# Kernel optimization log

Hardware: AMD Instinct MI355X
Metric: run time of the kernel (lower is better)

The kernel has to match this reference:

```python
import jax, jax.numpy as jnp
import numpy as np

N_NODES = 20000   # N
N_EDGES = 320000  # E (avg degree 16)
T_STEPS = 16      # T
IN_FEATS = 1      # F
HG = 64           # hidden_g
HT = 128          # hidden_t
LN_EPS = 1e-5


def _layer_norm(x, g, b):
    mu = jnp.mean(x, axis=-1, keepdims=True)
    var = jnp.mean((x - mu) ** 2, axis=-1, keepdims=True)
    return (x - mu) * jax.lax.rsqrt(var + LN_EPS) * g + b


def setup_inputs() -> dict:
    key = jax.random.key(0)
    k = jax.random.split(key, 16)
    r = lambda i, shape, s: jax.random.normal(k[i], shape, jnp.float32) * s
    return dict(
        x_seq=jax.random.normal(k[0], (1, T_STEPS, N_NODES, IN_FEATS), jnp.float32),
        edge_index=jax.random.randint(k[1], (2, N_EDGES), 0, N_NODES, dtype=jnp.int32),
        # SAGEConv layer 0: lin_l (aggregated neighbors, has bias) + lin_r (root)
        W_l0=r(2, (IN_FEATS, HG), 0.5), W_r0=r(3, (IN_FEATS, HG), 0.5), b0=jnp.zeros((HG,), jnp.float32),
        ln0_g=jnp.ones((HG,), jnp.float32), ln0_b=jnp.zeros((HG,), jnp.float32),
        # SAGEConv layer 1
        W_l1=r(4, (HG, HG), 0.1), W_r1=r(5, (HG, HG), 0.1), b1=jnp.zeros((HG,), jnp.float32),
        ln1_g=jnp.ones((HG,), jnp.float32), ln1_b=jnp.zeros((HG,), jnp.float32),
        # GRU (torch layout: gates r,z,n stacked along first dim)
        gru_Wih=r(6, (3 * HT, HG), 0.05), gru_Whh=r(7, (3 * HT, HT), 0.05),
        gru_bih=jnp.zeros((3 * HT,), jnp.float32), gru_bhh=jnp.zeros((3 * HT,), jnp.float32),
        # head
        head_W=r(8, (HT, 1), 0.05), head_b=jnp.zeros((1,), jnp.float32),
    )


def reference(x_seq, edge_index, W_l0, W_r0, b0, ln0_g, ln0_b,
              W_l1, W_r1, b1, ln1_g, ln1_b,
              gru_Wih, gru_Whh, gru_bih, gru_bhh, head_W, head_b):
    src, dst = edge_index[0], edge_index[1]
    # in-degree for mean aggregation (clamped to 1, like PyG mean aggr on isolated nodes)
    deg = jnp.clip(jax.ops.segment_sum(jnp.ones((N_EDGES,), jnp.float32), dst,
                                       num_segments=N_NODES), 1.0)[:, None]

    def sage(x, Wl, Wr, b):
        # mean over incoming neighbors, then lin_l(aggr) + lin_r(root)
        agg = jax.ops.segment_sum(x[src], dst, num_segments=N_NODES) / deg
        return agg @ Wl + x @ Wr + b

    def stack(xt):  # xt: (N, F) -> (N, HG); dropout is identity in eval mode
        h = jax.nn.relu(_layer_norm(sage(xt, W_l0, W_r0, b0), ln0_g, ln0_b))
        h = jax.nn.relu(_layer_norm(sage(h, W_l1, W_r1, b1), ln1_g, ln1_b))
        return h

    X = x_seq[0]  # (T, N, F), B == 1
    # scan over timesteps (matches the per-t Python loop, bounds peak memory)
    _, H = jax.lax.scan(lambda c, xt: (c, stack(xt)), None, X)  # H: (T, N, HG)

    def gru_step(h, xt):  # torch GRU cell; batch = N nodes
        gi = xt @ gru_Wih.T + gru_bih
        gh = h @ gru_Whh.T + gru_bhh
        ir, iz, inn = jnp.split(gi, 3, axis=-1)
        hr, hz, hn = jnp.split(gh, 3, axis=-1)
        r = jax.nn.sigmoid(ir + hr)
        z = jax.nn.sigmoid(iz + hz)
        n = jnp.tanh(inn + r * hn)
        return (1.0 - z) * n + z * h, None

    h0 = jnp.zeros((N_NODES, HT), x_seq.dtype)
    hT, _ = jax.lax.scan(gru_step, h0, H)
    y = (hT @ head_W + head_b)[:, 0]  # (N,)
    return y
```

## Files before the change

### kernel.cpp

```cpp
#include <hip/hip_runtime.h>
#include <math.h>

#define NN 20000
#define NE 320000
#define TS 16
#define HG 64
#define HTT 128
#define NG 384
#define LN_EPS 1e-5f
#define ASTR 1032

typedef __attribute__((ext_vector_type(8))) _Float16 f16x8;
typedef __attribute__((ext_vector_type(4))) float f32x4;

__device__ __forceinline__ float wave_sum64(float v) {
  #pragma unroll
  for (int off = 32; off > 0; off >>= 1) v += __shfl_xor(v, off, 64);
  return v;
}
__device__ __forceinline__ float quad_sum16(float v) {
  #pragma unroll
  for (int off = 1; off < 16; off <<= 1) v += __shfl_xor(v, off, 64);
  return v;
}
__device__ __forceinline__ float fast_sigmoid(float x) {
  return __builtin_amdgcn_rcpf(1.f + __expf(-x));
}
__device__ __forceinline__ float fast_tanh(float x) {
  float e = __expf(-2.f * fabsf(x));
  float th = (1.f - e) * __builtin_amdgcn_rcpf(1.f + e);
  return copysignf(th, x);
}

__global__ __launch_bounds__(256) void k_setup(
    const float* __restrict__ x_seq, float* __restrict__ xT,
    const float* __restrict__ Wih, _Float16* __restrict__ WihF,
    const float* __restrict__ Whh, _Float16* __restrict__ WhhF,
    const float* __restrict__ Wl1, const float* __restrict__ Wr1,
    _Float16* __restrict__ Wchi, _Float16* __restrict__ Wclo,
    const float* __restrict__ Wl0, const float* __restrict__ Wr0,
    const float* __restrict__ b0, const float* __restrict__ g0,
    const float* __restrict__ be0, float* __restrict__ P,
    int* __restrict__ cnt) {
  int gid = blockIdx.x * 256 + threadIdx.x;
  int stride = gridDim.x * 256;
  for (int i = gid; i < NN * TS; i += stride) {
    int t = i / NN, n = i - t * NN;
    xT[n * 16 + t] = x_seq[i];
  }
  for (int i = gid; i < NG * HG; i += stride) WihF[i] = (_Float16)Wih[i];
  for (int i = gid; i < NG * HTT; i += stride) WhhF[i] = (_Float16)Whh[i];
  for (int i = gid; i < HG * 128; i += stride) {
    int n = i >> 7, k = i & 127;
    float x = (k < HG) ? Wl1[k * HG + n] : Wr1[(k - HG) * HG + n];
    _Float16 h = (_Float16)x;
    Wchi[i] = h;
    Wclo[i] = (_Float16)(x - (float)h);
  }
  for (int i = gid; i < NN; i += stride) cnt[i] = 0;
  if (blockIdx.x == 0 && threadIdx.x < 64) {
    int f = threadIdx.x;
    float u = Wl0[f], v = Wr0[f], c = b0[f], g = g0[f];
    float um = wave_sum64(u) * (1.f / 64.f);
    float vm = wave_sum64(v) * (1.f / 64.f);
    float cm = wave_sum64(c) * (1.f / 64.f);
    float uc = u - um, vc = v - vm, cc = c - cm;
    float muu = wave_sum64(uc * uc) * (1.f / 64.f);
    float mvv = wave_sum64(vc * vc) * (1.f / 64.f);
    float mcc = wave_sum64(cc * cc) * (1.f / 64.f);
    float muv = wave_sum64(uc * vc) * (1.f / 64.f);
    float muc = wave_sum64(uc * cc) * (1.f / 64.f);
    float mvc = wave_sum64(vc * cc) * (1.f / 64.f);
    P[f] = uc * g; P[64 + f] = vc * g; P[128 + f] = cc * g; P[192 + f] = be0[f];
    if (f == 0) {
      P[256] = muu; P[257] = mvv; P[258] = mcc;
      P[259] = muv; P[260] = muc; P[261] = mvc;
    }
  }
}

__global__ void k_hist(const int* __restrict__ dst, int* cnt) {
  int e = blockIdx.x * blockDim.x + threadIdx.x;
  if (e < NE) atomicAdd(&cnt[dst[e]], 1);
}

__global__ void k_scan(int* cnt, int* row_ptr, float* deg_inv) {
  __shared__ int s[1024];
  const int PER = 20;
  int tid = threadIdx.x;
  int base = tid * PER;
  int vloc[PER], dloc[PER];
  int sum = 0;
  #pragma unroll
  for (int j = 0; j < PER; j++) {
    int n = base + j;
    int d = (n < NN) ? cnt[n] : 0;
    vloc[j] = sum;
    dloc[j] = d;
    sum += d;
  }
  s[tid] = sum;
  __syncthreads();
  for (int off = 1; off < 1024; off <<= 1) {
    int t = (tid >= off) ? s[tid - off] : 0;
    __syncthreads();
    s[tid] += t;
    __syncthreads();
  }
  int excl = s[tid] - sum;
  #pragma unroll
  for (int j = 0; j < PER; j++) {
    int n = base + j;
    if (n < NN) {
      int rp = excl + vloc[j];
      row_ptr[n] = rp;
      cnt[n] = rp;
      int d = dloc[j];
      deg_inv[n] = 1.0f / (float)((d > 1) ? d : 1);
    }
  }
  if (tid == 1023) row_ptr[NN] = s[1023];
}

__global__ void k_fill(const int* __restrict__ src, const int* __restrict__ dst,
                       int* cursor, int* col) {
  int e = blockIdx.x * blockDim.x + threadIdx.x;
  if (e < NE) {
    int p = atomicAdd(&cursor[dst[e]], 1);
    col[p] = src[e];
  }
}

__global__ __launch_bounds__(256) void k_h0_fused(
    const float* __restrict__ xT,
    const int* __restrict__ row_ptr, const int* __restrict__ col,
    const float* __restrict__ deg_inv,
    const float* __restrict__ P,
    _Float16* __restrict__ h0r) {
  int lane = threadIdx.x & 63;
  int n = blockIdx.x * 4 + (threadIdx.x >> 6);
  int grp = lane >> 4, tl = lane & 15;
  int beg = row_ptr[n];
  int deg = row_ptr[n + 1] - beg;
  float s0 = 0.f, s1 = 0.f;
  int iters = (deg + 7) >> 3;
  for (int it = 0; it < iters; it++) {
    int e0 = it * 8 + grp, e1 = it * 8 + 4 + grp;
    bool v0 = e0 < deg, v1 = e1 < deg;
    int i0 = v0 ? e0 : 0, i1 = v1 ? e1 : 0;
    int c0 = col[beg + i0];
    int c1 = col[beg + i1];
    float x0 = xT[c0 * 16 + tl];
    float x1 = xT[c1 * 16 + tl];
    s0 += v0 ? x0 : 0.f;
    s1 += v1 ? x1 : 0.f;
  }
  float s = s0 + s1;
  s += __shfl_xor(s, 16, 64);
  s += __shfl_xor(s, 32, 64);
  float aggv = s * deg_inv[n];
  float xv = xT[n * 16 + tl];
  float muu = P[256], mvv = P[257], mcc = P[258];
  float muv = P[259], muc = P[260], mvc = P[261];
  #pragma unroll
  for (int half = 0; half < 2; half++) {
    int c = lane + half * 64;
    int t = c >> 3, f8 = (c & 7) * 8;
    float a = __shfl(aggv, t, 64);
    float x = __shfl(xv, t, 64);
    float var = a * a * muu + x * x * mvv + mcc
              + 2.f * (a * x * muv + a * muc + x * mvc);
    float rstd = rsqrtf(var + LN_EPS);
    f16x8 o;
    #pragma unroll
    for (int j = 0; j < 8; j++) {
      int f = f8 + j;
      float d = a * P[f] + x * P[64 + f] + P[128 + f];
      o[j] = (_Float16)fmaxf(d * rstd + P[192 + f], 0.f);
    }
    *(f16x8*)&h0r[(size_t)n * 1024 + c * 8] = o;
  }
}

__global__ __launch_bounds__(256) void k_sage_fused(
    const _Float16* __restrict__ h0r,
    const int* __restrict__ row_ptr, const int* __restrict__ col,
    const float* __restrict__ deg_inv,
    const _Float16* __restrict__ Wchi, const _Float16* __restrict__ Wclo,
    const float* __restrict__ b1, const float* __restrict__ g1, const float* __restrict__ be1,
    _Float16* __restrict__ Ht_all) {
  __shared__ _Float16 aggL[16 * ASTR];
  int tid = threadIdx.x;
  int lane = tid & 63, wave = tid >> 6;
  int col16 = lane & 15, quad = lane >> 4;
  int m0 = blockIdx.x * 16;

  for (int i = 0; i < 4; i++) {
    int nl = wave * 4 + i;
    int n = m0 + nl;
    int beg = row_ptr[n];
    int deg = row_ptr[n + 1] - beg;
    const f16x8 z = {0,0,0,0,0,0,0,0};
    f16x8 aH0 = z, aH1 = z, aH2 = z, aH3 = z;
    f16x8 aL0 = z, aL1 = z, aL2 = z, aL3 = z;
    int e = 0;
    for (; e + 8 <= deg; e += 8) {
      int c0 = col[beg + e + 0], c1 = col[beg + e + 1];
      int c2 = col[beg + e + 2], c3 = col[beg + e + 3];
      int c4 = col[beg + e + 4], c5 = col[beg + e + 5];
      int c6 = col[beg + e + 6], c7 = col[beg + e + 7];
      const f16x8* p0 = (const f16x8*)(h0r + (size_t)c0 * 1024);
      const f16x8* p1 = (const f16x8*)(h0r + (size_t)c1 * 1024);
      const f16x8* p2 = (const f16x8*)(h0r + (size_t)c2 * 1024);
      const f16x8* p3 = (const f16x8*)(h0r + (size_t)c3 * 1024);
      const f16x8* p4 = (const f16x8*)(h0r + (size_t)c4 * 1024);
      const f16x8* p5 = (const f16x8*)(h0r + (size_t)c5 * 1024);
      const f16x8* p6 = (const f16x8*)(h0r + (size_t)c6 * 1024);
      const f16x8* p7 = (const f16x8*)(h0r + (size_t)c7 * 1024);
      f16x8 d0a = p0[lane], d0b = p0[lane + 64];
      f16x8 d1a = p1[lane], d1b = p1[lane + 64];
      f16x8 d2a = p2[lane], d2b = p2[lane + 64];
      f16x8 d3a = p3[lane], d3b = p3[lane + 64];
      f16x8 d4a = p4[lane], d4b = p4[lane + 64];
      f16x8 d5a = p5[lane], d5b = p5[lane + 64];
      f16x8 d6a = p6[lane], d6b = p6[lane + 64];
      f16x8 d7a = p7[lane], d7b = p7[lane + 64];
      aH0 += d0a; aL0 += d0b;
      aH1 += d1a; aL1 += d1b;
      aH2 += d2a; aL2 += d2b;
      aH3 += d3a; aL3 += d3b;
      aH0 += d4a; aL0 += d4b;
      aH1 += d5a; aL1 += d5b;
      aH2 += d6a; aL2 += d6b;
      aH3 += d7a; aL3 += d7b;
    }
    for (; e + 4 <= deg; e += 4) {
      int c0 = col[beg + e + 0], c1 = col[beg + e + 1];
      int c2 = col[beg + e + 2], c3 = col[beg + e + 3];
      const f16x8* p0 = (const f16x8*)(h0r + (size_t)c0 * 1024);
      const f16x8* p1 = (const f16x8*)(h0r + (size_t)c1 * 1024);
      const f16x8* p2 = (const f16x8*)(h0r + (size_t)c2 * 1024);
      const f16x8* p3 = (const f16x8*)(h0r + (size_t)c3 * 1024);
      f16x8 d0a = p0[lane], d0b = p0[lane + 64];
      f16x8 d1a = p1[lane], d1b = p1[lane + 64];
      f16x8 d2a = p2[lane], d2b = p2[lane + 64];
      f16x8 d3a = p3[lane], d3b = p3[lane + 64];
      aH0 += d0a; aL0 += d0b;
      aH1 += d1a; aL1 += d1b;
      aH2 += d2a; aL2 += d2b;
      aH3 += d3a; aL3 += d3b;
    }
    for (; e < deg; e++) {
      int c = col[beg + e];
      const f16x8* p = (const f16x8*)(h0r + (size_t)c * 1024);
      aH0 += p[lane]; aL0 += p[lane + 64];
    }
    float di = deg_inv[n];
    f16x8 o0, o1;
    #pragma unroll
    for (int j = 0; j < 8; j++) {
      o0[j] = (_Float16)((((float)aH0[j] + (float)aH1[j]) +
                          ((float)aH2[j] + (float)aH3[j])) * di);
      o1[j] = (_Float16)((((float)aL0[j] + (float)aL1[j]) +
                          ((float)aL2[j] + (float)aL3[j])) * di);
    }
    *(f16x8*)&aggL[nl * ASTR + lane * 8] = o0;
    *(f16x8*)&aggL[nl * ASTR + 512 + lane * 8] = o1;
  }
  __syncthreads();

  for (int ts = 0; ts < 4; ts++) {
    int t = wave * 4 + ts;
    f32x4 acc[4];
    #pragma unroll
    for (int nt = 0; nt < 4; nt++) acc[nt] = (f32x4){0.f, 0.f, 0.f, 0.f};

    #pragma unroll
    for (int kk = 0; kk < 2; kk++) {
      f16x8 ah = *(const f16x8*)&aggL[col16 * ASTR + t * 64 + kk * 32 + quad * 8];
      #pragma unroll
      for (int nt = 0; nt < 4; nt++) {
        int nf = nt * 16 + col16;
        f16x8 bh = *(const f16x8*)&Wchi[nf * 128 + kk * 32 + quad * 8];
        f16x8 bl = *(const f16x8*)&Wclo[nf * 128 + kk * 32 + quad * 8];
        acc[nt] = __builtin_amdgcn_mfma_f32_16x16x32_f16(ah, bh, acc[nt], 0, 0, 0);
        acc[nt] = __builtin_amdgcn_mfma_f32_16x16x32_f16(ah, bl, acc[nt], 0, 0, 0);
      }
    }
    #pragma unroll
    for (int kk = 0; kk < 2; kk++) {
      f16x8 ah = *(const f16x8*)&h0r[(size_t)(m0 + col16) * 1024 + t * 64 + kk * 32 + quad * 8];
      #pragma unroll
      for (int nt = 0; nt < 4; nt++) {
        int nf = nt * 16 + col16;
        f16x8 bh = *(const f16x8*)&Wchi[nf * 128 + 64 + kk * 32 + quad * 8];
        f16x8 bl = *(const f16x8*)&Wclo[nf * 128 + 64 + kk * 32 + quad * 8];
        acc[nt] = __builtin_amdgcn_mfma_f32_16x16x32_f16(ah, bh, acc[nt], 0, 0, 0);
        acc[nt] = __builtin_amdgcn_mfma_f32_16x16x32_f16(ah, bl, acc[nt], 0, 0, 0);
      }
    }

    float bias[4], gg[4], bb[4];
    #pragma unroll
    for (int nt = 0; nt < 4; nt++) {
      int nf = nt * 16 + col16;
      bias[nt] = b1[nf]; gg[nt] = g1[nf]; bb[nt] = be1[nf];
    }
    #pragma unroll
    for (int r = 0; r < 4; r++) {
      float v[4];
      #pragma unroll
      for (int nt = 0; nt < 4; nt++) v[nt] = acc[nt][r] + bias[nt];
      float s = (v[0] + v[1]) + (v[2] + v[3]);
      float mu = quad_sum16(s) * (1.f / 64.f);
      float sq = 0.f;
      #pragma unroll
      for (int nt = 0; nt < 4; nt++) { v[nt] -= mu; sq += v[nt] * v[nt]; }
      float var = quad_sum16(sq) * (1.f / 64.f);
      float rstd = rsqrtf(var + LN_EPS);
      int m = m0 + quad * 4 + r;
      size_t base = ((size_t)t * NN + m) * HG;
      #pragma unroll
      for (int nt = 0; nt < 4; nt++) {
        float o = fmaxf(v[nt] * rstd * gg[nt] + bb[nt], 0.f);
        Ht_all[base + nt * 16 + col16] = (_Float16)o;
      }
    }
  }
}

__global__ __launch_bounds__(256, 2) void k_gru_all(
    const _Float16* __restrict__ Ht_all,
    const _Float16* __restrict__ WihF,
    const _Float16* __restrict__ WhhF,
    const float* __restrict__ bih, const float* __restrict__ bhh,
    const float* __restrict__ headW, const float* __restrict__ headb,
    float* __restrict__ out) {
  __shared__ _Float16 WihL[NG * 64];
  __shared__ _Float16 hL[2][32 * 128];
  __shared__ float yL[4][32];

  int tid = threadIdx.x;
  int lane = tid & 63, wave = tid >> 6;
  int col16 = lane & 15, quad = lane >> 4;
  int m0 = blockIdx.x * 32;
  int gb = 2 * wave;

  for (int i = tid; i < NG * 8; i += 256) {
    int g = i >> 3, k8 = i & 7;
    *(f16x8*)&WihL[g * 64 + ((k8 + g) & 7) * 8] = *(const f16x8*)&WihF[g * 64 + k8 * 8];
  }
  for (int i = tid; i < 2 * 32 * 128; i += 256) hL[0][i] = (_Float16)0.f;

  int gts[6];
  #pragma unroll
  for (int t6 = 0; t6 < 6; t6++)
    gts[t6] = (t6 < 2) ? (gb + t6) : (t6 < 4) ? (8 + gb + t6 - 2) : (16 + gb + t6 - 4);

  f16x8 wgh[4][6];
  #pragma unroll
  for (int kk = 0; kk < 4; kk++)
    #pragma unroll
    for (int t6 = 0; t6 < 6; t6++)
      wgh[kk][t6] = *(const f16x8*)&WhhF[(size_t)(gts[t6] * 16 + col16) * HTT + kk * 32 + quad * 8];

  int jj[2]; float bR[2], bZ[2], bNi[2], bNh[2], hw[2];
  int waddr[2][4][2];
  #pragma unroll
  for (int js = 0; js < 2; js++) {
    int j = (gb + js) * 16 + col16;
    jj[js] = j;
    bR[js]  = bih[j] + bhh[j];
    bZ[js]  = bih[HTT + j] + bhh[HTT + j];
    bNi[js] = bih[2 * HTT + j];
    bNh[js] = bhh[2 * HTT + j];
    hw[js]  = headW[j];
    #pragma unroll
    for (int mt = 0; mt < 2; mt++)
      #pragma unroll
      for (int r = 0; r < 4; r++) {
        int row = mt * 16 + quad * 4 + r;
        waddr[mt][r][js] = row * 128 + (((j >> 3) + row) & 15) * 8 + (j & 7);
      }
  }
  float hreg[2][4][2];
  #pragma unroll
  for (int mt = 0; mt < 2; mt++)
    #pragma unroll
    for (int r = 0; r < 4; r++) { hreg[mt][r][0] = 0.f; hreg[mt][r][1] = 0.f; }

  size_t aoff[2][2];
  #pragma unroll
  for (int kk = 0; kk < 2; kk++)
    #pragma unroll
    for (int mt = 0; mt < 2; mt++)
      aoff[kk][mt] = (size_t)(m0 + mt * 16 + col16) * HG + kk * 32 + quad * 8;

  __syncthreads();

  for (int t = 0; t < TS; t++) {
    const _Float16* hcur = hL[t & 1];
    _Float16* hnxt = hL[(t + 1) & 1];

    f32x4 acc[8][2];
    #pragma unroll
    for (int a = 0; a < 8; a++) {
      acc[a][0] = (f32x4){0.f, 0.f, 0.f, 0.f};
      acc[a][1] = (f32x4){0.f, 0.f, 0.f, 0.f};
    }

    const _Float16* AH = Ht_all + (size_t)t * NN * HG;
    f16x8 gah[2][2];
    #pragma unroll
    for (int kk = 0; kk < 2; kk++)
      #pragma unroll
      for (int mt = 0; mt < 2; mt++)
        gah[kk][mt] = *(const f16x8*)&AH[aoff[kk][mt]];

    #pragma unroll
    for (int kk = 0; kk < 4; kk++) {
      f16x8 ah[2];
      #pragma unroll
      for (int mt = 0; mt < 2; mt++) {
        int row = mt * 16 + col16;
        int k8 = kk * 4 + quad;
        ah[mt] = *(const f16x8*)&hcur[row * 128 + ((k8 + row) & 15) * 8];
      }
      #pragma unroll
      for (int t6 = 0; t6 < 6; t6++) {
        int ai = (t6 < 4) ? t6 : t6 + 2;
        #pragma unroll
        for (int mt = 0; mt < 2; mt++)
          acc[ai][mt] = __builtin_amdgcn_mfma_f32_16x16x32_f16(ah[mt], wgh[kk][t6], acc[ai][mt], 0, 0, 0);
      }
    }
    #pragma unroll
    for (int kk = 0; kk < 2; kk++) {
      #pragma unroll
      for (int t6 = 0; t6 < 6; t6++) {
        int g = gts[t6] * 16 + col16;
        int k8 = kk * 4 + quad;
        f16x8 b = *(const f16x8*)&WihL[g * 64 + ((k8 + g) & 7) * 8];
        #pragma unroll
        for (int mt = 0; mt < 2; mt++)
          acc[t6][mt] = __builtin_amdgcn_mfma_f32_16x16x32_f16(gah[kk][mt], b, acc[t6][mt], 0, 0, 0);
      }
    }

    #pragma unroll
    for (int mt = 0; mt < 2; mt++) {
      #pragma unroll
      for (int r = 0; r < 4; r++) {
        #pragma unroll
        for (int js = 0; js < 2; js++) {
          float R  = acc[0 + js][mt][r] + bR[js];
          float Z  = acc[2 + js][mt][r] + bZ[js];
          float Ni = acc[4 + js][mt][r] + bNi[js];
          float Nh = acc[6 + js][mt][r] + bNh[js];
          float rg = fast_sigmoid(R);
          float zg = fast_sigmoid(Z);
          float nn = fast_tanh(Ni + rg * Nh);
          float hn = nn + zg * (hreg[mt][r][js] - nn);
          hreg[mt][r][js] = hn;
          hnxt[waddr[mt][r][js]] = (_Float16)hn;
        }
      }
    }
    __syncthreads();
  }

  #pragma unroll
  for (int mt = 0; mt < 2; mt++) {
    #pragma unroll
    for (int r = 0; r < 4; r++) {
      float py = hreg[mt][r][0] * hw[0] + hreg[mt][r][1] * hw[1];
      py = quad_sum16(py);
      if (col16 == 0) yL[wave][mt * 16 + quad * 4 + r] = py;
    }
  }
  __syncthreads();
  if (tid < 32)
    out[m0 + tid] = yL[0][tid] + yL[1][tid] + yL[2][tid] + yL[3][tid] + headb[0];
}

extern "C" void kernel_launch(void* const* d_in, const int* in_sizes, int n_in,
                              void* d_out, int out_size, void* d_ws, size_t ws_size,
                              hipStream_t stream) {
  const float* x_seq = (const float*)d_in[0];
  const int*   edge  = (const int*)d_in[1];
  const float* Wl0   = (const float*)d_in[2];
  const float* Wr0   = (const float*)d_in[3];
  const float* b0    = (const float*)d_in[4];
  const float* g0    = (const float*)d_in[5];
  const float* be0   = (const float*)d_in[6];
  const float* Wl1   = (const float*)d_in[7];
  const float* Wr1   = (const float*)d_in[8];
  const float* b1    = (const float*)d_in[9];
  const float* g1    = (const float*)d_in[10];
  const float* be1   = (const float*)d_in[11];
  const float* Wih   = (const float*)d_in[12];
  const float* Whh   = (const float*)d_in[13];
  const float* bih   = (const float*)d_in[14];
  const float* bhh   = (const float*)d_in[15];
  const float* headW = (const float*)d_in[16];
  const float* headb = (const float*)d_in[17];
  float* out = (float*)d_out;

  const int* srcp = edge;
  const int* dstp = edge + NE;

  char* ws = (char*)d_ws;
  size_t off = 0;
  auto alloc = [&](size_t bytes) -> void* {
    void* p = ws + off;
    off += (bytes + 255) & ~(size_t)255;
    return p;
  };
  int*   cnt     = (int*)alloc(NN * 4);
  int*   row_ptr = (int*)alloc((NN + 1) * 4);
  int*   col     = (int*)alloc(NE * 4);
  float* deg_inv = (float*)alloc(NN * 4);
  float* xT      = (float*)alloc((size_t)NN * TS * 4);
  float* P       = (float*)alloc(512 * 4);
  _Float16* h0r  = (_Float16*)alloc((size_t)NN * 1024 * 2);
  _Float16* Ht_all = (_Float16*)alloc((size_t)TS * NN * HG * 2);
  _Float16* WihF = (_Float16*)alloc((size_t)NG * HG * 2);
  _Float16* WhhF = (_Float16*)alloc((size_t)NG * HTT * 2);
  _Float16* Wchi = (_Float16*)alloc((size_t)HG * 128 * 2);
  _Float16* Wclo = (_Float16*)alloc((size_t)HG * 128 * 2);
  (void)ws_size; (void)in_sizes; (void)n_in; (void)out_size;

  k_setup<<<1250, 256, 0, stream>>>(x_seq, xT, Wih, WihF, Whh, WhhF,
                                    Wl1, Wr1, Wchi, Wclo,
                                    Wl0, Wr0, b0, g0, be0, P, cnt);
  k_hist<<<(NE + 255) / 256, 256, 0, stream>>>(dstp, cnt);
  k_scan<<<1, 1024, 0, stream>>>(cnt, row_ptr, deg_inv);
  k_fill<<<(NE + 255) / 256, 256, 0, stream>>>(srcp, dstp, cnt, col);
  k_h0_fused<<<NN / 4, 256, 0, stream>>>(xT, row_ptr, col, deg_inv, P, h0r);
  k_sage_fused<<<NN / 16, 256, 0, stream>>>(h0r, row_ptr, col, deg_inv,
                                            Wchi, Wclo, b1, g1, be1, Ht_all);
  k_gru_all<<<NN / 32, 256, 0, stream>>>(Ht_all, WihF, WhhF, bih, bhh,
                                         headW, headb, out);
}
```

Baseline: 396.5 us.

## Split SAGE layer-1 into XCD-partitioned gather and separate per-timestep MFMA kernel

The h0 activations are stored in eight feature-group slabs instead of one 2 KB row per node. A new gather kernel assigns each feature group to its own block stride (blockIdx & 7), so each XCD works on a 5 MB slab that can stay L2-resident during the random neighbor gather. The mean-aggregated result goes to a global aggX buffer, and a separate kernel gridded over (node block, timestep) does the MFMA, LayerNorm and ReLU. This trades the fused LDS path for an extra global write and read of aggX (about 40 MB) plus one more launch, in return for better cache locality in the gather.

```diff
diff --git a/kernel.cpp b/kernel.cpp
--- a/kernel.cpp
+++ b/kernel.cpp
@@ -8,7 +8,6 @@
 #define HTT 128
 #define NG 384
 #define LN_EPS 1e-5f
-#define ASTR 1032
 
 typedef __attribute__((ext_vector_type(8))) _Float16 f16x8;
 typedef __attribute__((ext_vector_type(4))) float f32x4;
@@ -136,7 +135,7 @@
     const int* __restrict__ row_ptr, const int* __restrict__ col,
     const float* __restrict__ deg_inv,
     const float* __restrict__ P,
-    _Float16* __restrict__ h0r) {
+    _Float16* __restrict__ h0x) {
   int lane = threadIdx.x & 63;
   int n = blockIdx.x * 4 + (threadIdx.x >> 6);
   int grp = lane >> 4, tl = lane & 15;
@@ -165,7 +164,7 @@
   #pragma unroll
   for (int half = 0; half < 2; half++) {
     int c = lane + half * 64;
-    int t = c >> 3, f8 = (c & 7) * 8;
+    int t = c >> 3, fg = c & 7, f8 = fg * 8;
     float a = __shfl(aggv, t, 64);
     float x = __shfl(xv, t, 64);
     float var = a * a * muu + x * x * mvv + mcc
@@ -178,147 +177,121 @@
       float d = a * P[f] + x * P[64 + f] + P[128 + f];
       o[j] = (_Float16)fmaxf(d * rstd + P[192 + f], 0.f);
     }
-    *(f16x8*)&h0r[(size_t)n * 1024 + c * 8] = o;
-  }
-}
-
-__global__ __launch_bounds__(256) void k_sage_fused(
-    const _Float16* __restrict__ h0r,
+    *(f16x8*)&h0x[((size_t)fg * NN + n) * 128 + t * 8] = o;
+  }
+}
+
+__global__ __launch_bounds__(256) void k_gather_xcd(
+    const _Float16* __restrict__ h0x,
     const int* __restrict__ row_ptr, const int* __restrict__ col,
     const float* __restrict__ deg_inv,
+    _Float16* __restrict__ aggX) {
+  int fg = blockIdx.x & 7;
+  int nb = blockIdx.x >> 3;
+  int lane = threadIdx.x & 63, wave = threadIdx.x >> 6;
+  int grp = lane >> 4, tl = lane & 15;
+  const _Float16* h0f = h0x + (size_t)fg * NN * 128;
+  _Float16* aggf = aggX + (size_t)fg * NN * 128;
+  const f16x8 z = {0,0,0,0,0,0,0,0};
+  for (int i = 0; i < 16; i++) {
+    int n = nb * 64 + wave * 16 + i;
+    if (n >= NN) return;
+    int beg = row_ptr[n];
+    int deg = row_ptr[n + 1] - beg;
+    f16x8 aE = z, aO = z;
+    int iters = (deg + 7) >> 3;
+    for (int it = 0; it < iters; it++) {
+      int e0 = it * 8 + grp, e1 = it * 8 + 4 + grp;
+      bool v0 = e0 < deg, v1 = e1 < deg;
+      int c0 = col[beg + (v0 ? e0 : 0)];
+      int c1 = col[beg + (v1 ? e1 : 0)];
+      f16x8 d0 = *(const f16x8*)&h0f[(size_t)c0 * 128 + tl * 8];
+      f16x8 d1 = *(const f16x8*)&h0f[(size_t)c1 * 128 + tl * 8];
+      d0 = v0 ? d0 : z;
+      d1 = v1 ? d1 : z;
+      aE += d0;
+      aO += d1;
+    }
+    float s[8];
+    #pragma unroll
+    for (int j = 0; j < 8; j++) s[j] = (float)aE[j] + (float)aO[j];
+    #pragma unroll
+    for (int j = 0; j < 8; j++) {
+      s[j] += __shfl_xor(s[j], 16, 64);
+      s[j] += __shfl_xor(s[j], 32, 64);
+    }
+    if (grp == 0) {
+      float di = deg_inv[n];
+      f16x8 o;
+      #pragma unroll
+      for (int j = 0; j < 8; j++) o[j] = (_Float16)(s[j] * di);
+      *(f16x8*)&aggf[(size_t)n * 128 + tl * 8] = o;
+    }
+  }
+}
+
+__global__ __launch_bounds__(256) void k_sage_mm(
+    const _Float16* __restrict__ aggX, const _Float16* __restrict__ h0x,
     const _Float16* __restrict__ Wchi, const _Float16* __restrict__ Wclo,
     const float* __restrict__ b1, const float* __restrict__ g1, const float* __restrict__ be1,
     _Float16* __restrict__ Ht_all) {
-  __shared__ _Float16 aggL[16 * ASTR];
-  int tid = threadIdx.x;
-  int lane = tid & 63, wave = tid >> 6;
+  int t = blockIdx.y;
+  int lane = threadIdx.x & 63, wave = threadIdx.x >> 6;
   int col16 = lane & 15, quad = lane >> 4;
-  int m0 = blockIdx.x * 16;
-
-  for (int i = 0; i < 4; i++) {
-    int nl = wave * 4 + i;
-    int n = m0 + nl;
-    int beg = row_ptr[n];
-    int deg = row_ptr[n + 1] - beg;
-    const f16x8 z = {0,0,0,0,0,0,0,0};
-    f16x8 aH0 = z, aH1 = z, aH2 = z, aH3 = z;
-    f16x8 aL0 = z, aL1 = z, aL2 = z, aL3 = z;
-    int e = 0;
-    for (; e + 8 <= deg; e += 8) {
-      int c0 = col[beg + e + 0], c1 = col[beg + e + 1];
-      int c2 = col[beg + e + 2], c3 = col[beg + e + 3];
-      int c4 = col[beg + e + 4], c5 = col[beg + e + 5];
-      int c6 = col[beg + e + 6], c7 = col[beg + e + 7];
-      const f16x8* p0 = (const f16x8*)(h0r + (size_t)c0 * 1024);
-      const f16x8* p1 = (const f16x8*)(h0r + (size_t)c1 * 1024);
-      const f16x8* p2 = (const f16x8*)(h0r + (size_t)c2 * 1024);
-      const f16x8* p3 = (const f16x8*)(h0r + (size_t)c3 * 1024);
-      const f16x8* p4 = (const f16x8*)(h0r + (size_t)c4 * 1024);
-      const f16x8* p5 = (const f16x8*)(h0r + (size_t)c5 * 1024);
-      const f16x8* p6 = (const f16x8*)(h0r + (size_t)c6 * 1024);
-      const f16x8* p7 = (const f16x8*)(h0r + (size_t)c7 * 1024);
-      f16x8 d0a = p0[lane], d0b = p0[lane + 64];
-      f16x8 d1a = p1[lane], d1b = p1[lane + 64];
-      f16x8 d2a = p2[lane], d2b = p2[lane + 64];
-      f16x8 d3a = p3[lane], d3b = p3[lane + 64];
-      f16x8 d4a = p4[lane], d4b = p4[lane + 64];
-      f16x8 d5a = p5[lane], d5b = p5[lane + 64];
-      f16x8 d6a = p6[lane], d6b = p6[lane + 64];
-      f16x8 d7a = p7[lane], d7b = p7[lane + 64];
-      aH0 += d0a; aL0 += d0b;
-      aH1 += d1a; aL1 += d1b;
-      aH2 += d2a; aL2 += d2b;
-      aH3 += d3a; aL3 += d3b;
-      aH0 += d4a; aL0 += d4b;
-      aH1 += d5a; aL1 += d5b;
-      aH2 += d6a; aL2 += d6b;
-      aH3 += d7a; aL3 += d7b;
-    }
-    for (; e + 4 <= deg; e += 4) {
-      int c0 = col[beg + e + 0], c1 = col[beg + e + 1];
-      int c2 = col[beg + e + 2], c3 = col[beg + e + 3];
-      const f16x8* p0 = (const f16x8*)(h0r + (size_t)c0 * 1024);
-      const f16x8* p1 = (const f16x8*)(h0r + (size_t)c1 * 1024);
-      const f16x8* p2 = (const f16x8*)(h0r + (size_t)c2 * 1024);
-      const f16x8* p3 = (const f16x8*)(h0r + (size_t)c3 * 1024);
-      f16x8 d0a = p0[lane], d0b = p0[lane + 64];
-      f16x8 d1a = p1[lane], d1b = p1[lane + 64];
-      f16x8 d2a = p2[lane], d2b = p2[lane + 64];
-      f16x8 d3a = p3[lane], d3b = p3[lane + 64];
-      aH0 += d0a; aL0 += d0b;
-      aH1 += d1a; aL1 += d1b;
-      aH2 += d2a; aL2 += d2b;
-      aH3 += d3a; aL3 += d3b;
-    }
-    for (; e < deg; e++) {
-      int c = col[beg + e];
-      const f16x8* p = (const f16x8*)(h0r + (size_t)c * 1024);
-      aH0 += p[lane]; aL0 += p[lane + 64];
-    }
-    float di = deg_inv[n];
-    f16x8 o0, o1;
-    #pragma unroll
-    for (int j = 0; j < 8; j++) {
-      o0[j] = (_Float16)((((float)aH0[j] + (float)aH1[j]) +
-                          ((float)aH2[j] + (float)aH3[j])) * di);
-      o1[j] = (_Float16)((((float)aL0[j] + (float)aL1[j]) +
-                          ((float)aL2[j] + (float)aL3[j])) * di);
-    }
-    *(f16x8*)&aggL[nl * ASTR + lane * 8] = o0;
-    *(f16x8*)&aggL[nl * ASTR + 512 + lane * 8] = o1;
-  }
-  __syncthreads();
-
-  for (int ts = 0; ts < 4; ts++) {
-    int t = wave * 4 + ts;
-    f32x4 acc[4];
-    #pragma unroll
-    for (int nt = 0; nt < 4; nt++) acc[nt] = (f32x4){0.f, 0.f, 0.f, 0.f};
-
-    #pragma unroll
-    for (int kk = 0; kk < 2; kk++) {
-      f16x8 ah = *(const f16x8*)&aggL[col16 * ASTR + t * 64 + kk * 32 + quad * 8];
-      #pragma unroll
-      for (int nt = 0; nt < 4; nt++) {
-        int nf = nt * 16 + col16;
-        f16x8 bh = *(const f16x8*)&Wchi[nf * 128 + kk * 32 + quad * 8];
-        f16x8 bl = *(const f16x8*)&Wclo[nf * 128 + kk * 32 + quad * 8];
-        acc[nt] = __builtin_amdgcn_mfma_f32_16x16x32_f16(ah, bh, acc[nt], 0, 0, 0);
-        acc[nt] = __builtin_amdgcn_mfma_f32_16x16x32_f16(ah, bl, acc[nt], 0, 0, 0);
-      }
-    }
-    #pragma unroll
-    for (int kk = 0; kk < 2; kk++) {
-      f16x8 ah = *(const f16x8*)&h0r[(size_t)(m0 + col16) * 1024 + t * 64 + kk * 32 + quad * 8];
-      #pragma unroll
-      for (int nt = 0; nt < 4; nt++) {
-        int nf = nt * 16 + col16;
-        f16x8 bh = *(const f16x8*)&Wchi[nf * 128 + 64 + kk * 32 + quad * 8];
-        f16x8 bl = *(const f16x8*)&Wclo[nf * 128 + 64 + kk * 32 + quad * 8];
-        acc[nt] = __builtin_amdgcn_mfma_f32_16x16x32_f16(ah, bh, acc[nt], 0, 0, 0);
-        acc[nt] = __builtin_amdgcn_mfma_f32_16x16x32_f16(ah, bl, acc[nt], 0, 0, 0);
-      }
-    }
-
-    float bias[4], gg[4], bb[4];
+  int m0 = blockIdx.x * 64 + wave * 16;
+  int arow = m0 + col16; if (arow >= NN) arow = NN - 1;
+
+  f32x4 acc[4];
+  #pragma unroll
+  for (int nt = 0; nt < 4; nt++) acc[nt] = (f32x4){0.f, 0.f, 0.f, 0.f};
+
+  #pragma unroll
+  for (int kk = 0; kk < 2; kk++) {
+    int fg = kk * 4 + quad;
+    f16x8 ah = *(const f16x8*)&aggX[((size_t)fg * NN + arow) * 128 + t * 8];
     #pragma unroll
     for (int nt = 0; nt < 4; nt++) {
       int nf = nt * 16 + col16;
-      bias[nt] = b1[nf]; gg[nt] = g1[nf]; bb[nt] = be1[nf];
-    }
-    #pragma unroll
-    for (int r = 0; r < 4; r++) {
-      float v[4];
-      #pragma unroll
-      for (int nt = 0; nt < 4; nt++) v[nt] = acc[nt][r] + bias[nt];
-      float s = (v[0] + v[1]) + (v[2] + v[3]);
-      float mu = quad_sum16(s) * (1.f / 64.f);
-      float sq = 0.f;
-      #pragma unroll
-      for (int nt = 0; nt < 4; nt++) { v[nt] -= mu; sq += v[nt] * v[nt]; }
-      float var = quad_sum16(sq) * (1.f / 64.f);
-      float rstd = rsqrtf(var + LN_EPS);
-      int m = m0 + quad * 4 + r;
+      f16x8 bh = *(const f16x8*)&Wchi[nf * 128 + kk * 32 + quad * 8];
+      f16x8 bl = *(const f16x8*)&Wclo[nf * 128 + kk * 32 + quad * 8];
+      acc[nt] = __builtin_amdgcn_mfma_f32_16x16x32_f16(ah, bh, acc[nt], 0, 0, 0);
+      acc[nt] = __builtin_amdgcn_mfma_f32_16x16x32_f16(ah, bl, acc[nt], 0, 0, 0);
+    }
+  }
+  #pragma unroll
+  for (int kk = 0; kk < 2; kk++) {
+    int fg = kk * 4 + quad;
+    f16x8 ah = *(const f16x8*)&h0x[((size_t)fg * NN + arow) * 128 + t * 8];
+    #pragma unroll
+    for (int nt = 0; nt < 4; nt++) {
+      int nf = nt * 16 + col16;
+      f16x8 bh = *(const f16x8*)&Wchi[nf * 128 + 64 + kk * 32 + quad * 8];
+      f16x8 bl = *(const f16x8*)&Wclo[nf * 128 + 64 + kk * 32 + quad * 8];
+      acc[nt] = __builtin_amdgcn_mfma_f32_16x16x32_f16(ah, bh, acc[nt], 0, 0, 0);
+      acc[nt] = __builtin_amdgcn_mfma_f32_16x16x32_f16(ah, bl, acc[nt], 0, 0, 0);
+    }
+  }
+
+  float bias[4], gg[4], bb[4];
+  #pragma unroll
+  for (int nt = 0; nt < 4; nt++) {
+    int nf = nt * 16 + col16;
+    bias[nt] = b1[nf]; gg[nt] = g1[nf]; bb[nt] = be1[nf];
+  }
+  #pragma unroll
+  for (int r = 0; r < 4; r++) {
+    float v[4];
+    #pragma unroll
+    for (int nt = 0; nt < 4; nt++) v[nt] = acc[nt][r] + bias[nt];
+    float s = (v[0] + v[1]) + (v[2] + v[3]);
+    float mu = quad_sum16(s) * (1.f / 64.f);
+    float sq = 0.f;
+    #pragma unroll
+    for (int nt = 0; nt < 4; nt++) { v[nt] -= mu; sq += v[nt] * v[nt]; }
+    float var = quad_sum16(sq) * (1.f / 64.f);
+    float rstd = rsqrtf(var + LN_EPS);
+    int m = m0 + quad * 4 + r;
+    if (m < NN) {
       size_t base = ((size_t)t * NN + m) * HG;
       #pragma unroll
       for (int nt = 0; nt < 4; nt++) {
@@ -522,7 +495,8 @@
   float* deg_inv = (float*)alloc(NN * 4);
   float* xT      = (float*)alloc((size_t)NN * TS * 4);
   float* P       = (float*)alloc(512 * 4);
-  _Float16* h0r  = (_Float16*)alloc((size_t)NN * 1024 * 2);
+  _Float16* h0x  = (_Float16*)alloc((size_t)8 * NN * 128 * 2);
+  _Float16* aggX = (_Float16*)alloc((size_t)8 * NN * 128 * 2);
   _Float16* Ht_all = (_Float16*)alloc((size_t)TS * NN * HG * 2);
   _Float16* WihF = (_Float16*)alloc((size_t)NG * HG * 2);
   _Float16* WhhF = (_Float16*)alloc((size_t)NG * HTT * 2);
@@ -536,9 +510,11 @@
   k_hist<<<(NE + 255) / 256, 256, 0, stream>>>(dstp, cnt);
   k_scan<<<1, 1024, 0, stream>>>(cnt, row_ptr, deg_inv);
   k_fill<<<(NE + 255) / 256, 256, 0, stream>>>(srcp, dstp, cnt, col);
-  k_h0_fused<<<NN / 4, 256, 0, stream>>>(xT, row_ptr, col, deg_inv, P, h0r);
-  k_sage_fused<<<NN / 16, 256, 0, stream>>>(h0r, row_ptr, col, deg_inv,
-                                            Wchi, Wclo, b1, g1, be1, Ht_all);
+  k_h0_fused<<<NN / 4, 256, 0, stream>>>(xT, row_ptr, col, deg_inv, P, h0x);
+  k_gather_xcd<<<8 * ((NN + 63) / 64), 256, 0, stream>>>(h0x, row_ptr, col,
+                                                         deg_inv, aggX);
+  k_sage_mm<<<dim3((NN + 63) / 64, TS), 256, 0, stream>>>(aggX, h0x, Wchi, Wclo,
+                                                          b1, g1, be1, Ht_all);
   k_gru_all<<<NN / 32, 256, 0, stream>>>(Ht_all, WihF, WhhF, bih, bhh,
                                          headW, headb, out);
 }
```

Measured after the change: 469.8 us. +18.5%, slower.
